# Optimization experiments

Measured on AMD Instinct MI355X. Metric: run time of the kernel, lower is better.

Reference implementation:

```python
import jax, jax.numpy as jnp
import numpy as np


def binarize(x):
    # hard sign in forward, tanh surrogate gradient (STE)
    t = jnp.tanh(x)
    hard = jnp.where(x >= 0, jnp.ones_like(x), -jnp.ones_like(x))
    return jax.lax.stop_gradient(hard - t) + t


def round_ste(x):
    return x + jax.lax.stop_gradient(jnp.round(x) - x)


def binary_shift_scale(shift_param, lo=-8.0, hi=0.0):
    return 2.0 ** round_ste(jnp.clip(shift_param, lo, hi))


def setup_inputs() -> dict:
    key = jax.random.key(0)
    k1, k2 = jax.random.split(key)
    B, S, IN, OUT = 4, 2048, 4096, 16384
    x = jax.random.normal(k1, (B, S, IN), dtype=jnp.float32)
    weight = jax.random.normal(k2, (OUT, IN), dtype=jnp.float32) * 0.02
    threshold = jnp.zeros((OUT, 1), dtype=jnp.float32)
    shift_param = jnp.array(-4.5, dtype=jnp.float32)
    return {"x": x, "weight": weight, "threshold": threshold, "shift_param": shift_param}


def reference(x, weight, threshold, shift_param):
    xb = binarize(x)                               # [B,S,IN]
    wb = binarize(weight - threshold)              # [OUT,IN]
    out = jnp.einsum('bsi,oi->bso', xb, wb)        # dense GEMM on +/-1 values
    return out * binary_shift_scale(shift_param)   # pow2 shift scale
```

## Files before the change

### kernel.cpp

```cpp
#include <hip/hip_runtime.h>
#include <stdint.h>

#define M_ROWS 8192
#define N_COLS 16384
#define K_ELEMS 4096
#define KW 128
#define LDS_STRIDE 20

typedef int i32x4  __attribute__((ext_vector_type(4)));
typedef int i32x16 __attribute__((ext_vector_type(16)));

typedef const __attribute__((address_space(1))) void* gptr_t;
typedef __attribute__((address_space(3))) void*       lptr_t;

__device__ __forceinline__ void gload_lds16(const void* g, void* l) {
    __builtin_amdgcn_global_load_lds((gptr_t)g, (lptr_t)l, 16, 0, 0);
}

__global__ void conv_x_i8(const float4* __restrict__ x, uint32_t* __restrict__ o,
                          int n4) {
    int i = blockIdx.x * blockDim.x + threadIdx.x;
    int st = gridDim.x * blockDim.x;
    for (; i < n4; i += st) {
        float4 v = x[i];
        uint32_t b0 = (v.x >= 0.0f) ? 0x01u : 0xFFu;
        uint32_t b1 = (v.y >= 0.0f) ? 0x01u : 0xFFu;
        uint32_t b2 = (v.z >= 0.0f) ? 0x01u : 0xFFu;
        uint32_t b3 = (v.w >= 0.0f) ? 0x01u : 0xFFu;
        o[i] = b0 | (b1 << 8) | (b2 << 16) | (b3 << 24);
    }
}

__global__ void conv_w_i8(const float4* __restrict__ w, const float* __restrict__ thr,
                          uint32_t* __restrict__ o, int n4) {
    int i = blockIdx.x * blockDim.x + threadIdx.x;
    int st = gridDim.x * blockDim.x;
    for (; i < n4; i += st) {
        float t = thr[i >> 10];
        float4 v = w[i];
        uint32_t b0 = (v.x - t >= 0.0f) ? 0x01u : 0xFFu;
        uint32_t b1 = (v.y - t >= 0.0f) ? 0x01u : 0xFFu;
        uint32_t b2 = (v.z - t >= 0.0f) ? 0x01u : 0xFFu;
        uint32_t b3 = (v.w - t >= 0.0f) ? 0x01u : 0xFFu;
        o[i] = b0 | (b1 << 8) | (b2 << 16) | (b3 << 24);
    }
}

__launch_bounds__(256, 3)
__global__ void bgemm_i8(const char* __restrict__ A,
                         const char* __restrict__ B,
                         const float* __restrict__ shift,
                         float* __restrict__ out) {
    __shared__ __align__(16) char As[2][128 * 64];
    __shared__ __align__(16) char Bs[2][128 * 64];

    const int tid  = threadIdx.x;
    const int lane = tid & 63;
    const int wid  = tid >> 6;
    const int wx   = wid & 1;
    const int wy   = wid >> 1;
    const int bm   = blockIdx.y * 128;
    const int bn   = blockIdx.x * 128;

    const char* gA[2];
    const char* gB[2];
    int lofs[2];
    #pragma unroll
    for (int j = 0; j < 2; ++j) {
        int c  = wid * 2 + j;
        int li = c * 64 + lane;
        int r  = li >> 2;
        int s  = (li & 3) ^ ((r >> 1) & 3);
        gA[j]   = A + (size_t)(bm + r) * K_ELEMS + s * 16;
        gB[j]   = B + (size_t)(bn + r) * K_ELEMS + s * 16;
        lofs[j] = c * 1024;
    }

    const int l31 = lane & 31, hi = lane >> 5;
    int aOff[2][2], bOff[2][2];
    #pragma unroll
    for (int t = 0; t < 2; ++t) {
        int Rm = wy * 64 + t * 32 + l31;
        int Rn = wx * 64 + t * 32 + l31;
        #pragma unroll
        for (int ks = 0; ks < 2; ++ks) {
            aOff[t][ks] = Rm * 64 + (((ks * 2 + hi) ^ ((Rm >> 1) & 3)) << 4);
            bOff[t][ks] = Rn * 64 + (((ks * 2 + hi) ^ ((Rn >> 1) & 3)) << 4);
        }
    }

    i32x16 acc[2][2] = {};

    #pragma unroll
    for (int j = 0; j < 2; ++j) {
        gload_lds16(gA[j], &As[0][lofs[j]]);
        gload_lds16(gB[j], &Bs[0][lofs[j]]);
    }
    __syncthreads();

    const int NT = K_ELEMS / 64;
    #pragma unroll 2
    for (int t = 0; t < NT; ++t) {
        const int cur = t & 1;
        if (t + 1 < NT) {
            const int kb = (t + 1) * 64;
            #pragma unroll
            for (int j = 0; j < 2; ++j) {
                gload_lds16(gA[j] + kb, &As[cur ^ 1][lofs[j]]);
                gload_lds16(gB[j] + kb, &Bs[cur ^ 1][lofs[j]]);
            }
        }
        #pragma unroll
        for (int ks = 0; ks < 2; ++ks) {
            i32x4 a0 = *(const i32x4*)(&As[cur][aOff[0][ks]]);
            i32x4 a1 = *(const i32x4*)(&As[cur][aOff[1][ks]]);
            i32x4 b0 = *(const i32x4*)(&Bs[cur][bOff[0][ks]]);
            i32x4 b1 = *(const i32x4*)(&Bs[cur][bOff[1][ks]]);
            acc[0][0] = __builtin_amdgcn_mfma_i32_32x32x32_i8(a0, b0, acc[0][0], 0, 0, 0);
            acc[0][1] = __builtin_amdgcn_mfma_i32_32x32x32_i8(a0, b1, acc[0][1], 0, 0, 0);
            acc[1][0] = __builtin_amdgcn_mfma_i32_32x32x32_i8(a1, b0, acc[1][0], 0, 0, 0);
            acc[1][1] = __builtin_amdgcn_mfma_i32_32x32x32_i8(a1, b1, acc[1][1], 0, 0, 0);
        }
        __syncthreads();
    }

    float sp    = shift[0];
    float rr    = rintf(fminf(fmaxf(sp, -8.0f), 0.0f));
    float scale = exp2f(rr);

    #pragma unroll
    for (int mt = 0; mt < 2; ++mt) {
        #pragma unroll
        for (int nt = 0; nt < 2; ++nt) {
            #pragma unroll
            for (int reg = 0; reg < 16; ++reg) {
                int row = bm + wy * 64 + mt * 32 + (reg & 3) + 8 * (reg >> 2) + 4 * hi;
                int col = bn + wx * 64 + nt * 32 + l31;
                out[(size_t)row * N_COLS + col] = scale * (float)acc[mt][nt][reg];
            }
        }
    }
}

__global__ void pack_x_kernel(const float4* __restrict__ x,
                              uint64_t* __restrict__ out, int nwaves) {
    int lane = threadIdx.x & 63;
    int gw = (blockIdx.x * blockDim.x + threadIdx.x) >> 6;
    int stride = (gridDim.x * blockDim.x) >> 6;
    for (int w = gw; w < nwaves; w += stride) {
        float4 v = x[(size_t)w * 64 + lane];
        uint64_t m0 = __ballot(v.x < 0.0f);
        uint64_t m1 = __ballot(v.y < 0.0f);
        uint64_t m2 = __ballot(v.z < 0.0f);
        uint64_t m3 = __ballot(v.w < 0.0f);
        uint64_t sel = (lane == 0) ? m0 : (lane == 1) ? m1 : (lane == 2) ? m2 : m3;
        if (lane < 4) out[(size_t)w * 4 + lane] = sel;
    }
}

__global__ void pack_w_kernel(const float4* __restrict__ wgt,
                              const float* __restrict__ thr,
                              uint64_t* __restrict__ out, int nwaves) {
    int lane = threadIdx.x & 63;
    int gw = (blockIdx.x * blockDim.x + threadIdx.x) >> 6;
    int stride = (gridDim.x * blockDim.x) >> 6;
    for (int w = gw; w < nwaves; w += stride) {
        size_t f4 = (size_t)w * 64 + lane;
        float t = thr[f4 >> 10];
        float4 v = wgt[f4];
        uint64_t m0 = __ballot(v.x - t < 0.0f);
        uint64_t m1 = __ballot(v.y - t < 0.0f);
        uint64_t m2 = __ballot(v.z - t < 0.0f);
        uint64_t m3 = __ballot(v.w - t < 0.0f);
        uint64_t sel = (lane == 0) ? m0 : (lane == 1) ? m1 : (lane == 2) ? m2 : m3;
        if (lane < 4) out[(size_t)w * 4 + lane] = sel;
    }
}

__launch_bounds__(256, 2)
__global__ void bgemm_kernel(const uint32_t* __restrict__ A,
                             const uint32_t* __restrict__ B,
                             const float* __restrict__ shift,
                             float* __restrict__ out) {
    __shared__ uint32_t As[128 * LDS_STRIDE];
    __shared__ uint32_t Bs[128 * LDS_STRIDE];

    const int tid = threadIdx.x;
    const int tx = tid & 15;
    const int ty = tid >> 4;
    const int bm = blockIdx.y * 128;
    const int bn = blockIdx.x * 128;

    const int r0 = tid >> 2, g0 = tid & 3;
    const int r1 = (tid + 256) >> 2, g1 = tid & 3;

    uint32_t acc[8][8];
    #pragma unroll
    for (int i = 0; i < 8; ++i)
        #pragma unroll
        for (int j = 0; j < 8; ++j) acc[i][j] = 0u;

    uint4 pa0, pa1, pb0, pb1;
    pa0 = *(const uint4*)&A[(size_t)(bm + r0) * KW + 0 + g0 * 4];
    pa1 = *(const uint4*)&A[(size_t)(bm + r1) * KW + 0 + g1 * 4];
    pb0 = *(const uint4*)&B[(size_t)(bn + r0) * KW + 0 + g0 * 4];
    pb1 = *(const uint4*)&B[(size_t)(bn + r1) * KW + 0 + g1 * 4];

    for (int kb = 0; kb < KW; kb += 16) {
        *(uint4*)&As[r0 * LDS_STRIDE + g0 * 4] = pa0;
        *(uint4*)&As[r1 * LDS_STRIDE + g1 * 4] = pa1;
        *(uint4*)&Bs[r0 * LDS_STRIDE + g0 * 4] = pb0;
        *(uint4*)&Bs[r1 * LDS_STRIDE + g1 * 4] = pb1;
        __syncthreads();

        if (kb + 16 < KW) {
            int kn = kb + 16;
            pa0 = *(const uint4*)&A[(size_t)(bm + r0) * KW + kn + g0 * 4];
            pa1 = *(const uint4*)&A[(size_t)(bm + r1) * KW + kn + g1 * 4];
            pb0 = *(const uint4*)&B[(size_t)(bn + r0) * KW + kn + g0 * 4];
            pb1 = *(const uint4*)&B[(size_t)(bn + r1) * KW + kn + g1 * 4];
        }

        #pragma unroll
        for (int g = 0; g < 4; ++g) {
            uint4 b[8];
            #pragma unroll
            for (int c = 0; c < 8; ++c)
                b[c] = *(const uint4*)&Bs[(tx + 16 * c) * LDS_STRIDE + g * 4];
            #pragma unroll
            for (int r = 0; r < 8; ++r) {
                uint4 a = *(const uint4*)&As[(ty + 16 * r) * LDS_STRIDE + g * 4];
                #pragma unroll
                for (int c = 0; c < 8; ++c) {
                    acc[r][c] += __popc(a.x ^ b[c].x);
                    acc[r][c] += __popc(a.y ^ b[c].y);
                    acc[r][c] += __popc(a.z ^ b[c].z);
                    acc[r][c] += __popc(a.w ^ b[c].w);
                }
            }
        }
        __syncthreads();
    }

    float sp = shift[0];
    float rr = rintf(fminf(fmaxf(sp, -8.0f), 0.0f));
    float scale = exp2f(rr);
    float base = (float)K_ELEMS * scale;
    float m2s = -2.0f * scale;

    #pragma unroll
    for (int i = 0; i < 8; ++i) {
        size_t rowoff = (size_t)(bm + ty + 16 * i) * (size_t)N_COLS + (size_t)bn;
        #pragma unroll
        for (int j = 0; j < 8; ++j) {
            out[rowoff + tx + 16 * j] = fmaf(m2s, (float)acc[i][j], base);
        }
    }
}

extern "C" void kernel_launch(void* const* d_in, const int* in_sizes, int n_in,
                              void* d_out, int out_size, void* d_ws, size_t ws_size,
                              hipStream_t stream) {
    const float* x     = (const float*)d_in[0];
    const float* w     = (const float*)d_in[1];
    const float* thr   = (const float*)d_in[2];
    const float* shift = (const float*)d_in[3];
    float* out = (float*)d_out;

    const size_t A_BYTES = (size_t)M_ROWS * K_ELEMS;
    const size_t B_BYTES = (size_t)N_COLS * K_ELEMS;

    if (ws_size >= A_BYTES + B_BYTES) {
        char* Ai8 = (char*)d_ws;
        char* Bi8 = Ai8 + A_BYTES;

        conv_x_i8<<<2048, 256, 0, stream>>>((const float4*)x, (uint32_t*)Ai8,
                                            (int)(A_BYTES / 4));
        conv_w_i8<<<2048, 256, 0, stream>>>((const float4*)w, thr, (uint32_t*)Bi8,
                                            (int)(B_BYTES / 4));

        dim3 grid(N_COLS / 128, M_ROWS / 128);
        bgemm_i8<<<grid, 256, 0, stream>>>(Ai8, Bi8, shift, out);
    } else {
        uint32_t* Apk = (uint32_t*)d_ws;
        uint32_t* Bpk = Apk + (size_t)M_ROWS * KW;

        pack_x_kernel<<<2048, 256, 0, stream>>>((const float4*)x, (uint64_t*)Apk,
                                                (M_ROWS * K_ELEMS) / 256);
        pack_w_kernel<<<4096, 256, 0, stream>>>((const float4*)w, thr, (uint64_t*)Bpk,
                                                (N_COLS * K_ELEMS) / 256);

        dim3 grid(N_COLS / 128, M_ROWS / 128);
        bgemm_kernel<<<grid, 256, 0, stream>>>(Apk, Bpk, shift, out);
    }
}
```

Measured before the change: 1.384 ms.

## Enlarge int8 GEMM tiles to 256x256x128 with staged prefetch and block swizzle

Replaces the 128x128x64 int8 MFMA GEMM with a 256x256 block tile over K steps of 128, run by 512 threads with 64 KB of double-buffered LDS per operand. Global-to-LDS loads are split into per-quarter stages interleaved with the MFMA phases, with barriers, setprio around the MFMA bursts, and an XOR swizzle on LDS rows. A swizzled 1D grid improves L2 reuse. The larger tiles cut global and LDS traffic per MFMA, at the cost of one block per CU and more registers, which limits occupancy and latency hiding.

Result: no change. 1.402 ms (+1.3%).

```diff
diff --git a/kernel.cpp b/kernel.cpp
--- a/kernel.cpp
+++ b/kernel.cpp
@@ -13,7 +13,7 @@
 typedef const __attribute__((address_space(1))) void* gptr_t;
 typedef __attribute__((address_space(3))) void*       lptr_t;
 
-__device__ __forceinline__ void gload_lds16(const void* g, void* l) {
+__device__ __forceinline__ void gl16(const char* g, char* l) {
     __builtin_amdgcn_global_load_lds((gptr_t)g, (lptr_t)l, 16, 0, 0);
 }
 
@@ -46,95 +46,132 @@
     }
 }
 
-__launch_bounds__(256, 3)
-__global__ void bgemm_i8(const char* __restrict__ A,
-                         const char* __restrict__ B,
-                         const float* __restrict__ shift,
-                         float* __restrict__ out) {
-    __shared__ __align__(16) char As[2][128 * 64];
-    __shared__ __align__(16) char Bs[2][128 * 64];
+__launch_bounds__(512, 1)
+__global__ void bgemm_i8_256(const char* __restrict__ A,
+                             const char* __restrict__ B,
+                             const float* __restrict__ shift,
+                             float* __restrict__ out) {
+    __shared__ __align__(16) char As[2][256 * 128];
+    __shared__ __align__(16) char Bs[2][256 * 128];
 
     const int tid  = threadIdx.x;
     const int lane = tid & 63;
     const int wid  = tid >> 6;
-    const int wx   = wid & 1;
-    const int wy   = wid >> 1;
-    const int bm   = blockIdx.y * 128;
-    const int bn   = blockIdx.x * 128;
-
-    const char* gA[2];
-    const char* gB[2];
-    int lofs[2];
-    #pragma unroll
-    for (int j = 0; j < 2; ++j) {
-        int c  = wid * 2 + j;
-        int li = c * 64 + lane;
-        int r  = li >> 2;
-        int s  = (li & 3) ^ ((r >> 1) & 3);
-        gA[j]   = A + (size_t)(bm + r) * K_ELEMS + s * 16;
-        gB[j]   = B + (size_t)(bn + r) * K_ELEMS + s * 16;
-        lofs[j] = c * 1024;
-    }
+    const int wx   = wid & 3;
+    const int wy   = wid >> 2;
+
+    const int bid = blockIdx.x;
+    const int swz = (bid & 7) * 256 + (bid >> 3);
+    const int bn  = (swz & 63) * 256;
+    const int bm  = (swz >> 6) * 256;
+
+    const float sp    = shift[0];
+    const float rr    = rintf(fminf(fmaxf(sp, -8.0f), 0.0f));
+    const float scale = exp2f(rr);
+    asm volatile("" :: "v"(scale));
+
+    const int rl = lane >> 3;
+    const int sl = lane & 7;
+    const char* gsrc[8];
+    #pragma unroll
+    for (int q = 0; q < 8; ++q) {
+        int ch = q & 3;
+        int rt = ch * 64 + wid * 8 + rl;
+        const char* bp = (q < 4) ? A : B;
+        int brow       = (q < 4) ? bm : bn;
+        gsrc[q] = bp + (size_t)(brow + rt) * K_ELEMS + ((sl ^ rl) << 4);
+    }
+    const int ldst_w = wid * 1024;
+
+#define STAGE(q, buf, koff) do {                                             \
+        char* _d = ((q) < 4) ? &As[(buf)][((q) & 3) * 8192 + ldst_w]         \
+                             : &Bs[(buf)][((q) & 3) * 8192 + ldst_w];        \
+        gl16(gsrc[q] + (koff), _d);                                          \
+    } while (0)
 
     const int l31 = lane & 31, hi = lane >> 5;
-    int aOff[2][2], bOff[2][2];
-    #pragma unroll
-    for (int t = 0; t < 2; ++t) {
-        int Rm = wy * 64 + t * 32 + l31;
-        int Rn = wx * 64 + t * 32 + l31;
-        #pragma unroll
-        for (int ks = 0; ks < 2; ++ks) {
-            aOff[t][ks] = Rm * 64 + (((ks * 2 + hi) ^ ((Rm >> 1) & 3)) << 4);
-            bOff[t][ks] = Rn * 64 + (((ks * 2 + hi) ^ ((Rn >> 1) & 3)) << 4);
-        }
-    }
-
-    i32x16 acc[2][2] = {};
-
-    #pragma unroll
-    for (int j = 0; j < 2; ++j) {
-        gload_lds16(gA[j], &As[0][lofs[j]]);
-        gload_lds16(gB[j], &Bs[0][lofs[j]]);
-    }
-    __syncthreads();
-
-    const int NT = K_ELEMS / 64;
+    int aBase[4], bBase[2];
+    #pragma unroll
+    for (int mt = 0; mt < 4; ++mt) {
+        int r = wy * 128 + mt * 32 + l31;
+        aBase[mt] = r * 128 + ((hi ^ (r & 7)) << 4);
+    }
+    #pragma unroll
+    for (int nt = 0; nt < 2; ++nt) {
+        int r = wx * 64 + nt * 32 + l31;
+        bBase[nt] = r * 128 + ((hi ^ (r & 7)) << 4);
+    }
+
+    i32x16 acc[4][2] = {};
+
+    STAGE(0, 0, 0); STAGE(1, 0, 0); STAGE(2, 0, 0); STAGE(3, 0, 0);
+    STAGE(4, 0, 0); STAGE(5, 0, 0); STAGE(6, 0, 0); STAGE(7, 0, 0);
+    STAGE(0, 1, 128); STAGE(1, 1, 128); STAGE(2, 1, 128); STAGE(3, 1, 128);
+    asm volatile("s_waitcnt vmcnt(4)" ::: "memory");
+    __builtin_amdgcn_s_barrier();
+    asm volatile("" ::: "memory");
+
+    const int NT = K_ELEMS / 128;
     #pragma unroll 2
     for (int t = 0; t < NT; ++t) {
         const int cur = t & 1;
-        if (t + 1 < NT) {
-            const int kb = (t + 1) * 64;
-            #pragma unroll
-            for (int j = 0; j < 2; ++j) {
-                gload_lds16(gA[j] + kb, &As[cur ^ 1][lofs[j]]);
-                gload_lds16(gB[j] + kb, &Bs[cur ^ 1][lofs[j]]);
+        const char* curA = &As[cur][0];
+        const char* curB = &Bs[cur][0];
+        const int koff1 = (t + 1) * 128;
+
+        #pragma unroll
+        for (int p = 0; p < 4; ++p) {
+            i32x4 af[4], bf[2];
+            #pragma unroll
+            for (int mt = 0; mt < 4; ++mt)
+                af[mt] = *(const i32x4*)(curA + (aBase[mt] ^ (p << 5)));
+            #pragma unroll
+            for (int nt = 0; nt < 2; ++nt)
+                bf[nt] = *(const i32x4*)(curB + (bBase[nt] ^ (p << 5)));
+            if (t + 1 < NT) {
+                if      (p == 0) STAGE(4, cur ^ 1, koff1);
+                else if (p == 1) STAGE(5, cur ^ 1, koff1);
+                else if (p == 2) STAGE(6, cur ^ 1, koff1);
+                else             STAGE(7, cur ^ 1, koff1);
             }
-        }
-        #pragma unroll
-        for (int ks = 0; ks < 2; ++ks) {
-            i32x4 a0 = *(const i32x4*)(&As[cur][aOff[0][ks]]);
-            i32x4 a1 = *(const i32x4*)(&As[cur][aOff[1][ks]]);
-            i32x4 b0 = *(const i32x4*)(&Bs[cur][bOff[0][ks]]);
-            i32x4 b1 = *(const i32x4*)(&Bs[cur][bOff[1][ks]]);
-            acc[0][0] = __builtin_amdgcn_mfma_i32_32x32x32_i8(a0, b0, acc[0][0], 0, 0, 0);
-            acc[0][1] = __builtin_amdgcn_mfma_i32_32x32x32_i8(a0, b1, acc[0][1], 0, 0, 0);
-            acc[1][0] = __builtin_amdgcn_mfma_i32_32x32x32_i8(a1, b0, acc[1][0], 0, 0, 0);
-            acc[1][1] = __builtin_amdgcn_mfma_i32_32x32x32_i8(a1, b1, acc[1][1], 0, 0, 0);
-        }
-        __syncthreads();
-    }
-
-    float sp    = shift[0];
-    float rr    = rintf(fminf(fmaxf(sp, -8.0f), 0.0f));
-    float scale = exp2f(rr);
-
-    #pragma unroll
-    for (int mt = 0; mt < 2; ++mt) {
+            asm volatile("" ::: "memory");
+            __builtin_amdgcn_s_barrier();
+            asm volatile("" ::: "memory");
+            __builtin_amdgcn_s_setprio(1);
+            #pragma unroll
+            for (int mt = 0; mt < 4; ++mt)
+                #pragma unroll
+                for (int nt = 0; nt < 2; ++nt)
+                    acc[mt][nt] = __builtin_amdgcn_mfma_i32_32x32x32_i8(
+                        af[mt], bf[nt], acc[mt][nt], 0, 0, 0);
+            __builtin_amdgcn_s_setprio(0);
+            asm volatile("" ::: "memory");
+            __builtin_amdgcn_s_barrier();
+            asm volatile("" ::: "memory");
+        }
+
+        if (t + 2 < NT) {
+            const int koff2 = (t + 2) * 128;
+            STAGE(0, cur, koff2); STAGE(1, cur, koff2);
+            STAGE(2, cur, koff2); STAGE(3, cur, koff2);
+            asm volatile("s_waitcnt vmcnt(4)" ::: "memory");
+            __builtin_amdgcn_s_barrier();
+            asm volatile("" ::: "memory");
+        } else if (t + 1 < NT) {
+            asm volatile("s_waitcnt vmcnt(0)" ::: "memory");
+            __builtin_amdgcn_s_barrier();
+            asm volatile("" ::: "memory");
+        }
+    }
+#undef STAGE
+
+    #pragma unroll
+    for (int mt = 0; mt < 4; ++mt) {
         #pragma unroll
         for (int nt = 0; nt < 2; ++nt) {
             #pragma unroll
             for (int reg = 0; reg < 16; ++reg) {
-                int row = bm + wy * 64 + mt * 32 + (reg & 3) + 8 * (reg >> 2) + 4 * hi;
+                int row = bm + wy * 128 + mt * 32 + (reg & 3) + 8 * (reg >> 2) + 4 * hi;
                 int col = bn + wx * 64 + nt * 32 + l31;
                 out[(size_t)row * N_COLS + col] = scale * (float)acc[mt][nt][reg];
             }
@@ -279,8 +316,7 @@
         conv_w_i8<<<2048, 256, 0, stream>>>((const float4*)w, thr, (uint32_t*)Bi8,
                                             (int)(B_BYTES / 4));
 
-        dim3 grid(N_COLS / 128, M_ROWS / 128);
-        bgemm_i8<<<grid, 256, 0, stream>>>(Ai8, Bi8, shift, out);
+        bgemm_i8_256<<<2048, 512, 0, stream>>>(Ai8, Bi8, shift, out);
     } else {
         uint32_t* Apk = (uint32_t*)d_ws;
         uint32_t* Bpk = Apk + (size_t)M_ROWS * KW;
```
